# Performance work log

Hardware: AMD Instinct MI355X
Metric: run time of the kernel (lower is better)

Reference implementation:

```python
import jax, jax.numpy as jnp
import numpy as np

B, L, H, NH, HD, IT = 16, 512, 256, 8, 32, 2
NEG = -9e15


def _ln(x, g, b):
    m = x.mean(-1, keepdims=True)
    v = ((x - m) ** 2).mean(-1, keepdims=True)
    return (x - m) / jnp.sqrt(v + 1e-5) * g + b


def setup_inputs() -> dict:
    key = jax.random.key(0)
    ks = jax.random.split(key, 12)

    def nrm(k, shape, fan_in):
        return jax.random.normal(k, shape, dtype=jnp.float32) / np.float32(np.sqrt(fan_in))

    return {
        "data": jax.random.normal(ks[0], (B, L, H), jnp.float32),
        "gat_WQ_w": nrm(ks[1], (NH, H, H), H),
        "gat_WQ_b": jnp.zeros((NH, H), jnp.float32),
        "gat_a1": nrm(ks[2], (NH, 3 * H), 3 * H),
        "gat_a2": nrm(ks[3], (NH, 3 * H), 3 * H),
        "gat_fc_w": nrm(ks[4], (NH, 3 * H, HD), 3 * H),
        "gat_fc_b": jnp.zeros((NH, HD), jnp.float32),
        "norm_g": jnp.ones((IT, H), jnp.float32),
        "norm_b": jnp.zeros((IT, H), jnp.float32),
        "sq_w": nrm(ks[5], (IT, NH * HD, H), H),
        "sq_b": jnp.zeros((IT, NH * HD), jnp.float32),
        "sk_w": nrm(ks[6], (IT, NH * HD, H), H),
        "sk_b": jnp.zeros((IT, NH * HD), jnp.float32),
        "so_w": nrm(ks[7], (IT, H, NH * HD), NH * HD),
        "so_b": jnp.zeros((IT, H), jnp.float32),
        "fc_w": nrm(ks[8], (NH * HD, H), NH * HD),
        "fc_b": jnp.zeros((H,), jnp.float32),
        "mask": jax.random.randint(ks[9], (B, L), 0, 2, jnp.int32),
        "edge_matrix": jax.random.randint(ks[10], (B, L, L), 0, 2, jnp.int32),
    }


def _gat_head(xn, ax, adj_pos, Wq, bq, a1, a2, Fw, Fb):
    # xn: [B,L,H] normalized nodes; ax: [B,L,2H] interleaved (r_embs, relay)
    h = jnp.concatenate([xn @ Wq.T + bq, ax], axis=-1)  # [B,L,3H]
    # decomposed a^T [h_i ; h_j] = a1.h_i + a2.h_j  (avoids O(N^2*6H) concat)
    ei = h @ a1  # [B,L]
    ej = h @ a2  # [B,L]
    e = jax.nn.leaky_relu(ei[:, :, None] + ej[:, None, :], 0.2)  # [B,L,L]
    att = jax.nn.softmax(jnp.where(adj_pos, e, NEG), axis=2)
    hp = jnp.einsum('bij,bjd->bid', att, h)  # [B,L,3H]
    return jax.nn.elu(hp @ Fw + Fb)  # [B,L,HD]


def _forward(data, gat_WQ_w, gat_WQ_b, gat_a1, gat_a2, gat_fc_w, gat_fc_b,
             norm_g, norm_b, sq_w, sq_b, sk_w, sk_b, so_w, so_b, fc_w, fc_b,
             mask, edge_matrix):
    pad = mask == 0                                   # True at padding positions
    smask = jnp.concatenate([jnp.zeros((B, 1), bool), pad], axis=1)  # [B,L+1]
    adj_pos = edge_matrix > 0
    nodes = data                                      # [B,L,H]
    relay = data.mean(axis=1)                         # [B,H]
    gat = jax.vmap(_gat_head, in_axes=(None, None, None, 0, 0, 0, 0, 0, 0))
    scale = np.float32(1.0 / np.sqrt(HD))

    for i in range(IT):
        xn = _ln(nodes, norm_g[i], norm_b[i])
        # torch views [B,H,2,L] as [B,2H,L]: features interleave (r_embs, relay)
        ax = jnp.stack([data, jnp.broadcast_to(relay[:, None, :], (B, L, H))],
                       axis=-1).reshape(B, L, 2 * H)
        heads = gat(xn, ax, adj_pos, gat_WQ_w, gat_WQ_b, gat_a1, gat_a2,
                    gat_fc_w, gat_fc_b)               # [NH,B,L,HD]
        temp = jnp.transpose(heads, (1, 2, 0, 3)).reshape(B, L, NH * HD)
        nodes = nodes + jax.nn.leaky_relu(temp @ fc_w + fc_b, 0.01)
        # star attention (MSA2); note original uses v = k (WV unused)
        y = jnp.concatenate([relay[:, None, :], nodes], axis=1)   # [B,L+1,H]
        q = (relay @ sq_w[i].T + sq_b[i]).reshape(B, NH, HD)
        k = (y @ sk_w[i].T + sk_b[i]).transpose(0, 2, 1).reshape(B, NH, HD, L + 1)
        v = jnp.swapaxes(k, 2, 3)                                  # [B,NH,L+1,HD]
        pre = jnp.einsum('bnd,bndl->bnl', q, k) * scale
        pre = jnp.where(smask[:, None, :], -jnp.inf, pre)
        al = jax.nn.softmax(pre, axis=2)
        att = jnp.einsum('bnl,bnld->bnd', al, v).reshape(B, NH * HD)
        relay = jax.nn.leaky_relu(att @ so_w[i].T + so_b[i], 0.01)
        nodes = jnp.where(pad[:, :, None], 0.0, nodes)
    return nodes, relay


def reference(data, gat_WQ_w, gat_WQ_b, gat_a1, gat_a2, gat_fc_w, gat_fc_b,
              norm_g, norm_b, sq_w, sq_b, sk_w, sk_b, so_w, so_b, fc_w, fc_b,
              mask, edge_matrix):
    return _forward(data, gat_WQ_w, gat_WQ_b, gat_a1, gat_a2, gat_fc_w, gat_fc_b,
                    norm_g, norm_b, sq_w, sq_b, sk_w, sk_b, so_w, so_b, fc_w, fc_b,
                    mask, edge_matrix)
```

## Files before the change

kernel.cpp:

```cpp
#include <hip/hip_runtime.h>
#include <hip/hip_bf16.h>
#include <math.h>

#define BB 16
#define LL 512
#define HH 256
#define NHEAD 8
#define HDIM 32
#define LP1 513
#define NODES_ELEMS (BB*LL*HH)

typedef __attribute__((ext_vector_type(8))) short bf16x8;
typedef __attribute__((ext_vector_type(4))) float f32x4;

__device__ __forceinline__ unsigned short f2bf(float f) {
  union { float f; unsigned u; } x; x.f = f;
  unsigned r = x.u + 0x7fffu + ((x.u >> 16) & 1u);
  return (unsigned short)(r >> 16);
}
__device__ __forceinline__ float bf2f(unsigned short u) {
  union { unsigned u; float f; } x; x.u = (unsigned)u << 16; return x.f;
}

__global__ __launch_bounds__(256) void mega_prep_kernel(
    const float* __restrict__ data, const int* __restrict__ edge,
    const float* __restrict__ fc_w, const float* __restrict__ fcw,
    const float* __restrict__ sk_w, const float* __restrict__ sq_w,
    const float* __restrict__ so_w, const float* __restrict__ WQw,
    const float* __restrict__ WQb, const float* __restrict__ a1,
    const float* __restrict__ a2,
    unsigned short* __restrict__ datab, unsigned char* __restrict__ ep,
    unsigned short* __restrict__ fcwT, unsigned short* __restrict__ Bcat,
    unsigned short* __restrict__ skwb, float* __restrict__ sqT,
    float* __restrict__ soT, float* __restrict__ rpart,
    float* __restrict__ w1, float* __restrict__ w2,
    float* __restrict__ c1, float* __restrict__ c2,
    float* __restrict__ bqf, float* __restrict__ a1o, float* __restrict__ a2o) {
  int blk = blockIdx.x, t = threadIdx.x;
  if (blk < 2048) {
    int idx = blk * 1024 + t;
#pragma unroll
    for (int u = 0; u < 4; u++) { datab[idx] = f2bf(data[idx]); idx += 256; }
  } else if (blk < 4096) {
    int row = (blk - 2048) * 4 + (t >> 6);
    int lane = t & 63;
    const int* adj = edge + ((size_t)row << 9);
    unsigned v = 0;
#pragma unroll
    for (int u = 0; u < 8; u++) v |= (adj[lane + 64 * u] > 0 ? 1u : 0u) << u;
    ep[((size_t)row << 6) + lane] = (unsigned char)v;
  } else if (blk < 5120) {
    int b2 = blk - 4096;
    if (b2 < 256) {
      int idx = b2 * 256 + t;
      int o = idx >> 8, k = idx & 255;
      fcwT[idx] = f2bf(fc_w[k * 256 + o]);
    } else if (b2 < 512) {
      int idx = (b2 - 256) * 256 + t;
      int n = idx >> 13, d = (idx >> 8) & 31, c = idx & 255;
      Bcat[((size_t)n * 32 + d) * 512 + 256 + c] =
          f2bf(fcw[((size_t)n * 768 + 256 + 2 * c) * 32 + d]);
    } else {
      int idx = (b2 - 512) * 256 + t;
      skwb[idx] = f2bf(sk_w[idx]);
    }
  } else if (blk < 6144) {
    int q = blk - 5120;
    int which = q >> 8;
    const float* in = (which < 2) ? sq_w + which * 65536 : so_w + (which - 2) * 65536;
    float* out = (which < 2) ? sqT + which * 65536 : soT + (which - 2) * 65536;
    int idx = (q & 255) * 256 + t;
    int r = idx >> 8, c = idx & 255;
    out[c * 256 + r] = in[idx];
  } else if (blk < 6272) {
    int q = blk - 6144;
    int b = q >> 3, ch = q & 7;
    float s = 0.f;
    const float* p = data + ((size_t)b * 512 + ch * 64) * 256 + t;
    for (int l = 0; l < 64; l++) s += p[(size_t)l * 256];
    rpart[(size_t)q * 256 + t] = s;
  } else if (blk < 6280) {
    int n = blk - 6272;
    float s1 = 0.f, s2 = 0.f;
    for (int c = 0; c < 256; c++) {
      float wv = WQw[((size_t)(n * 256 + c)) * 256 + t];
      s1 = fmaf(a1[n * 768 + c], wv, s1);
      s2 = fmaf(a2[n * 768 + c], wv, s2);
    }
    w1[n * 256 + t] = s1;
    w2[n * 256 + t] = s2;
    if (t < 32) {
      float s = 0.f;
      for (int c = 0; c < 256; c++)
        s = fmaf(WQb[n * 256 + c], fcw[((size_t)n * 768 + c) * 32 + t], s);
      bqf[n * 32 + t] = s;
    }
    __shared__ float r1[256], r2[256];
    r1[t] = a1[n * 768 + t] * WQb[n * 256 + t];
    r2[t] = a2[n * 768 + t] * WQb[n * 256 + t];
    __syncthreads();
    for (int o = 128; o; o >>= 1) {
      if (t < o) { r1[t] += r1[t + o]; r2[t] += r2[t + o]; }
      __syncthreads();
    }
    if (t == 0) { c1[n] = r1[0]; c2[n] = r2[0]; }
  } else {
    int n = blk - 6280;
    a1o[n * 256 + t] = a1[n * 768 + 256 + 2 * t];
    a2o[n * 256 + t] = a2[n * 768 + 256 + 2 * t];
  }
}

__global__ __launch_bounds__(256) void bcat_m1_kernel(const float* __restrict__ WQw,
                                                      const float* __restrict__ fcw,
                                                      unsigned short* __restrict__ Bcat) {
  __shared__ float wq_s[256][16];
  __shared__ float fw_s[256][32];
  int n = blockIdx.x >> 4, kt = blockIdx.x & 15;
  int t = threadIdx.x;
#pragma unroll
  for (int i = 0; i < 16; i++) {
    int c = i * 16 + (t >> 4), kk = t & 15;
    wq_s[c][kk] = WQw[(size_t)n * 65536 + c * 256 + kt * 16 + kk];
  }
#pragma unroll
  for (int i = 0; i < 32; i++) {
    int idx = i * 256 + t;
    fw_s[idx >> 5][idx & 31] = fcw[(size_t)n * 24576 + idx];
  }
  __syncthreads();
  int kloc = t >> 4, dp = t & 15;
  float a0 = 0.f, a1v = 0.f;
  for (int c = 0; c < 256; c++) {
    float wv = wq_s[c][kloc];
    a0 = fmaf(wv, fw_s[c][dp * 2], a0);
    a1v = fmaf(wv, fw_s[c][dp * 2 + 1], a1v);
  }
  int k = kt * 16 + kloc;
  Bcat[((size_t)n * 32 + dp * 2) * 512 + k] = f2bf(a0);
  Bcat[((size_t)n * 32 + dp * 2 + 1) * 512 + k] = f2bf(a1v);
}

__device__ __forceinline__ void rarf_tail(
    int n, int b, int t, const float* rel,
    const float* __restrict__ a1, const float* __restrict__ a2,
    const float* __restrict__ fcw, const float* __restrict__ fcb,
    const float* __restrict__ bqf,
    float* __restrict__ ra1, float* __restrict__ ra2, float* __restrict__ rf,
    float* red1, float* red2, float* pf_s) {
  int lane = t & 63, w = t >> 6;
  float p1 = rel[t] * a1[n * 768 + 257 + 2 * t];
  float p2 = rel[t] * a2[n * 768 + 257 + 2 * t];
#pragma unroll
  for (int o = 32; o; o >>= 1) { p1 += __shfl_xor(p1, o); p2 += __shfl_xor(p2, o); }
  if (lane == 0) { red1[w] = p1; red2[w] = p2; }
  int d = t & 31, seg = t >> 5;
  float pf = 0.f;
  for (int u = 0; u < 32; u++) {
    int k = seg * 32 + u;
    pf = fmaf(rel[k], fcw[((size_t)n * 768 + 257 + 2 * k) * 32 + d], pf);
  }
  pf_s[seg * 33 + d] = pf;
  __syncthreads();
  if (t == 0) {
    ra1[n * 16 + b] = red1[0] + red1[1] + red1[2] + red1[3];
    ra2[n * 16 + b] = red2[0] + red2[1] + red2[2] + red2[3];
  }
  if (t < 32) {
    float s = 0.f;
    for (int gg = 0; gg < 8; gg++) s += pf_s[gg * 33 + t];
    rf[((size_t)n * 16 + b) * 32 + t] = s + fcb[n * 32 + t] + bqf[n * 32 + t];
  }
}

__global__ __launch_bounds__(256) void relay_rarf_kernel(
    const float* __restrict__ rpart,
    const unsigned short* __restrict__ skw0, const float* __restrict__ skb0,
    const float* __restrict__ a1, const float* __restrict__ a2,
    const float* __restrict__ fcw, const float* __restrict__ fcb,
    const float* __restrict__ bqf,
    float* __restrict__ relay, unsigned short* __restrict__ ktb,
    float* __restrict__ ra1, float* __restrict__ ra2, float* __restrict__ rf) {
  __shared__ float rel[256];
  __shared__ float red1[4], red2[4];
  __shared__ float pf_s[8 * 33];
  int n = blockIdx.x >> 4, b = blockIdx.x & 15;
  int t = threadIdx.x;
  float s = 0.f;
#pragma unroll
  for (int ch = 0; ch < 8; ch++) s += rpart[((size_t)(b * 8 + ch)) * 256 + t];
  s *= (1.0f / 512.0f);
  rel[t] = s;
  __syncthreads();
  if (n == 0) {
    relay[b * 256 + t] = s;
    float acc = 0.f;
    for (int k = 0; k < 256; k++) acc = fmaf(rel[k], bf2f(skw0[(size_t)t * 256 + k]), acc);
    ktb[((size_t)b * LP1) * 256 + t] = f2bf(acc + skb0[t]);
  }
  rarf_tail(n, b, t, rel, a1, a2, fcw, fcb, bqf, ra1, ra2, rf, red1, red2, pf_s);
}

__global__ __launch_bounds__(256) void so_rarf_kernel(
    const float* __restrict__ atts,
    const float* __restrict__ soT_it, const float* __restrict__ sob_it,
    const unsigned short* __restrict__ skw_nx, const float* __restrict__ skb_nx,
    const float* __restrict__ a1, const float* __restrict__ a2,
    const float* __restrict__ fcw, const float* __restrict__ fcb,
    const float* __restrict__ bqf, int do_extras,
    float* __restrict__ relay, unsigned short* __restrict__ ktb,
    float* __restrict__ ra1, float* __restrict__ ra2, float* __restrict__ rf) {
  int n = blockIdx.x >> 4, b = blockIdx.x & 15;
  if (!do_extras && n > 0) return;
  __shared__ float xr[256];
  __shared__ float rel[256];
  __shared__ float red1[4], red2[4];
  __shared__ float pf_s[8 * 33];
  int t = threadIdx.x;
  xr[t] = atts[b * 256 + t];
  __syncthreads();
  float acc = 0.f;
  for (int k = 0; k < 256; k++) acc = fmaf(xr[k], soT_it[(size_t)k * 256 + t], acc);
  float v = acc + sob_it[t];
  v = v > 0.f ? v : 0.01f * v;
  rel[t] = v;
  __syncthreads();
  if (n == 0) relay[b * 256 + t] = v;
  if (!do_extras) return;
  if (n == 0) {
    float a2v = 0.f;
    for (int k = 0; k < 256; k++) a2v = fmaf(rel[k], bf2f(skw_nx[(size_t)t * 256 + k]), a2v);
    ktb[((size_t)b * LP1) * 256 + t] = f2bf(a2v + skb_nx[t]);
  }
  rarf_tail(n, b, t, rel, a1, a2, fcw, fcb, bqf, ra1, ra2, rf, red1, red2, pf_s);
}

__global__ __launch_bounds__(256) void lnei_kernel(const float* __restrict__ src,
                                                   const unsigned short* __restrict__ datab,
                                                   const float* __restrict__ g,
                                                   const float* __restrict__ bb,
                                                   const float* __restrict__ w1,
                                                   const float* __restrict__ w2,
                                                   const float* __restrict__ a1o,
                                                   const float* __restrict__ a2o,
                                                   const float* __restrict__ c1,
                                                   const float* __restrict__ c2,
                                                   const float* __restrict__ ra1,
                                                   const float* __restrict__ ra2,
                                                   unsigned short* __restrict__ xnb,
                                                   float* __restrict__ ei,
                                                   float* __restrict__ ej) {
  int r = blockIdx.x * 4 + (threadIdx.x >> 6);
  int b = r >> 9;
  int lane = threadIdx.x & 63;
  float x[4], dv[4];
#pragma unroll
  for (int u = 0; u < 4; u++) {
    int c = lane + 64 * u;
    x[u] = src[(size_t)r * 256 + c];
    dv[u] = bf2f(datab[(size_t)r * 256 + c]);
  }
  float s = x[0] + x[1] + x[2] + x[3];
#pragma unroll
  for (int o = 32; o; o >>= 1) s += __shfl_xor(s, o);
  float mean = s * (1.0f / 256.0f);
  float v = 0.f;
#pragma unroll
  for (int u = 0; u < 4; u++) { x[u] -= mean; v = fmaf(x[u], x[u], v); }
#pragma unroll
  for (int o = 32; o; o >>= 1) v += __shfl_xor(v, o);
  float rstd = rsqrtf(v * (1.0f / 256.0f) + 1e-5f);
  float xv[4];
#pragma unroll
  for (int u = 0; u < 4; u++) {
    int c = lane + 64 * u;
    xv[u] = x[u] * rstd * g[c] + bb[c];
    xnb[(size_t)r * 256 + c] = f2bf(xv[u]);
  }
  float s1a[8], s2a[8];
#pragma unroll
  for (int n = 0; n < 8; n++) {
    float s1 = 0.f, s2 = 0.f;
#pragma unroll
    for (int u = 0; u < 4; u++) {
      int c = lane + 64 * u;
      s1 = fmaf(xv[u], w1[n * 256 + c], s1);
      s1 = fmaf(dv[u], a1o[n * 256 + c], s1);
      s2 = fmaf(xv[u], w2[n * 256 + c], s2);
      s2 = fmaf(dv[u], a2o[n * 256 + c], s2);
    }
    s1a[n] = s1; s2a[n] = s2;
  }
#pragma unroll
  for (int o = 32; o; o >>= 1) {
#pragma unroll
    for (int n = 0; n < 8; n++) {
      s1a[n] += __shfl_xor(s1a[n], o);
      s2a[n] += __shfl_xor(s2a[n], o);
    }
  }
  if (lane == 0) {
#pragma unroll
    for (int n = 0; n < 8; n++) {
      ei[n * 8192 + r] = s1a[n] + c1[n] + ra1[n * 16 + b];
      ej[n * 8192 + r] = s2a[n] + c2[n] + ra2[n * 16 + b];
    }
  }
}

__global__ __launch_bounds__(256) void g_gemm_kernel(
    const unsigned short* __restrict__ A1, const unsigned short* __restrict__ A2,
    const unsigned short* __restrict__ Bcat, unsigned short* __restrict__ GT) {
  int tileN = blockIdx.x * 64;
  int tileM = blockIdx.y * 128;
  int t = threadIdx.x;
  int wv = t >> 6, lane = t & 63;
  int lo = lane & 15, quad = lane >> 4;
  int rowBase0 = tileM + wv * 32;
  const unsigned short* ap1[2];
  const unsigned short* ap2[2];
#pragma unroll
  for (int rt = 0; rt < 2; rt++) {
    int arow = rowBase0 + rt * 16 + lo;
    ap1[rt] = A1 + (size_t)arow * 256 + quad * 8;
    ap2[rt] = A2 + (size_t)arow * 256 + quad * 8;
  }
  f32x4 acc[2][4] = {};
  for (int k0 = 0; k0 < 512; k0 += 32) {
    bf16x8 af[2];
#pragma unroll
    for (int rt = 0; rt < 2; rt++)
      af[rt] = (k0 < 256) ? *(const bf16x8*)(ap1[rt] + k0)
                          : *(const bf16x8*)(ap2[rt] + k0 - 256);
#pragma unroll
    for (int ct = 0; ct < 4; ct++) {
      bf16x8 bf_ = *(const bf16x8*)(Bcat + (size_t)(tileN + ct * 16 + lo) * 512 + k0 + quad * 8);
#pragma unroll
      for (int rt = 0; rt < 2; rt++)
        acc[rt][ct] = __builtin_amdgcn_mfma_f32_16x16x32_bf16(af[rt], bf_, acc[rt][ct], 0, 0, 0);
    }
  }
#pragma unroll
  for (int rt = 0; rt < 2; rt++) {
#pragma unroll
    for (int ct = 0; ct < 4; ct++) {
      int co = tileN + ct * 16 + lo;
      int n = co >> 5, d = co & 31;
      int jrow = rowBase0 + rt * 16 + quad * 4;
      int b2 = jrow >> 9, jj = jrow & 511;
      ushort4 pk;
      pk.x = f2bf(acc[rt][ct][0]);
      pk.y = f2bf(acc[rt][ct][1]);
      pk.z = f2bf(acc[rt][ct][2]);
      pk.w = f2bf(acc[rt][ct][3]);
      *(ushort4*)&GT[(((size_t)(n * 16 + b2) * 32 + d) << 9) + jj] = pk;
    }
  }
}

__global__ __launch_bounds__(256) void gat_agg_kernel(
    const unsigned short* __restrict__ GT,
    const float* __restrict__ ei, const float* __restrict__ ej,
    const unsigned char* __restrict__ ep,
    const float* __restrict__ rf,
    unsigned short* __restrict__ tempb) {
  __shared__ unsigned short W[32][512];
  __shared__ float denom_s[32];
  int blk = blockIdx.x;
  int n = blk >> 8;
  int b = (blk >> 4) & 15;
  int i0 = (blk & 15) << 5;
  int t = threadIdx.x;
  int wv = t >> 6, lane = t & 63;
  int lo = lane & 15, quad = lane >> 4;

  const float* ejrow = ej + n * 8192 + b * 512;
  float ejv[8];
#pragma unroll
  for (int u = 0; u < 8; u++) ejv[u] = ejrow[lane + 64 * u];
  float mm = ejv[0];
#pragma unroll
  for (int u = 1; u < 8; u++) mm = fmaxf(mm, ejv[u]);
#pragma unroll
  for (int o = 32; o; o >>= 1) mm = fmaxf(mm, __shfl_xor(mm, o));

  for (int rr = 0; rr < 8; rr++) {
    int row = wv * 8 + rr;
    float eiv = ei[n * 8192 + b * 512 + i0 + row];
    float M = eiv + mm;
    M = M > 0.f ? M : 0.2f * M;
    unsigned pb = ep[(((size_t)(b * 512 + i0 + row)) << 6) + lane];
    int rx = (row & 7) << 3;
#pragma unroll
    for (int u = 0; u < 8; u++) {
      float e = eiv + ejv[u];
      e = e > 0.f ? e : 0.2f * e;
      float w = ((pb >> u) & 1) ? __expf(e - M) : 0.f;
      int col = lane + 64 * u;
      W[row][((col >> 3 << 3) ^ rx) + (col & 7)] = f2bf(w);
    }
  }
  __syncthreads();

  int rt = wv >> 1, dh = wv & 1;
  int arow = rt * 16 + lo;
  int rx = arow & 7;
  const unsigned short* gtb = GT + (((size_t)(n * 16 + b) * 32) << 9);
  bf16x8 bones;
  {
    short ov = (lo == 0) ? (short)0x3F80 : (short)0;
#pragma unroll
    for (int j = 0; j < 8; j++) bones[j] = ov;
  }
  f32x4 acc = {}, accd = {};
  for (int k0 = 0; k0 < 512; k0 += 32) {
    int chunk = (k0 >> 3) + quad;
    bf16x8 a0 = *(const bf16x8*)&W[arow][(chunk ^ rx) << 3];
    bf16x8 bf_ = *(const bf16x8*)(gtb + (((size_t)(dh * 16 + lo)) << 9) + k0 + quad * 8);
    acc = __builtin_amdgcn_mfma_f32_16x16x32_bf16(a0, bf_, acc, 0, 0, 0);
    if (dh == 0)
      accd = __builtin_amdgcn_mfma_f32_16x16x32_bf16(a0, bones, accd, 0, 0, 0);
  }
  if (dh == 0 && lo == 0) {
#pragma unroll
    for (int r = 0; r < 4; r++) denom_s[rt * 16 + quad * 4 + r] = accd[r];
  }
  __syncthreads();
  int d = dh * 16 + lo;
  float base = rf[((size_t)n * 16 + b) * 32 + d];
#pragma unroll
  for (int r = 0; r < 4; r++) {
    int row = rt * 16 + quad * 4 + r;
    float inv = 1.0f / fmaxf(denom_s[row], 1e-35f);
    float v = acc[r] * inv + base;
    v = v > 0.f ? v : expm1f(v);
    tempb[((size_t)(b * 512 + i0 + row)) * 256 + n * 32 + d] = f2bf(v);
  }
}

__global__ __launch_bounds__(256) void fc_kt_kernel(
    const unsigned short* __restrict__ tempb,
    const unsigned short* __restrict__ fcwT,
    const float* __restrict__ fc_b,
    const unsigned short* __restrict__ skw_it,
    const float* __restrict__ skb_it,
    const int* __restrict__ mask,
    const float* __restrict__ resid,
    float* __restrict__ nodes,
    unsigned short* __restrict__ ktb) {
  __shared__ unsigned short tmp[32][264];
  int blk = blockIdx.x;
  int b = blk >> 4;
  int i0 = (blk & 15) << 5;
  int t = threadIdx.x;
  int wv = t >> 6, lane = t & 63;
  int lo = lane & 15, quad = lane >> 4;
  int ch = wv >> 1, rt2 = wv & 1;

  const unsigned short* arow_p = tempb + ((size_t)(b * 512 + i0 + rt2 * 16 + lo)) * 256 + quad * 8;
  f32x4 facc[8] = {};
  for (int k0 = 0; k0 < 256; k0 += 32) {
    bf16x8 a0 = *(const bf16x8*)(arow_p + k0);
#pragma unroll
    for (int ct = 0; ct < 8; ct++) {
      int co = ch * 128 + ct * 16 + lo;
      bf16x8 bf_ = *(const bf16x8*)(fcwT + (size_t)co * 256 + k0 + quad * 8);
      facc[ct] = __builtin_amdgcn_mfma_f32_16x16x32_bf16(a0, bf_, facc[ct], 0, 0, 0);
    }
  }
#pragma unroll
  for (int ct = 0; ct < 8; ct++) {
    int co = ch * 128 + ct * 16 + lo;
    float bv = fc_b[co];
#pragma unroll
    for (int r = 0; r < 4; r++) {
      int row = rt2 * 16 + quad * 4 + r;
      int grow = b * 512 + i0 + row;
      float v = facc[ct][r] + bv;
      v = v > 0.f ? v : 0.01f * v;
      v = (mask[grow] != 0) ? resid[(size_t)grow * 256 + co] + v : 0.f;
      nodes[(size_t)grow * 256 + co] = v;
      tmp[row][co] = f2bf(v);
    }
  }
  __syncthreads();

  f32x4 kacc[8] = {};
  for (int k0 = 0; k0 < 256; k0 += 32) {
    bf16x8 a0 = *(const bf16x8*)&tmp[rt2 * 16 + lo][k0 + quad * 8];
#pragma unroll
    for (int ct = 0; ct < 8; ct++) {
      int co = ch * 128 + ct * 16 + lo;
      bf16x8 bf_ = *(const bf16x8*)(skw_it + (size_t)co * 256 + k0 + quad * 8);
      kacc[ct] = __builtin_amdgcn_mfma_f32_16x16x32_bf16(a0, bf_, kacc[ct], 0, 0, 0);
    }
  }
#pragma unroll
  for (int ct = 0; ct < 8; ct++) {
    int co = ch * 128 + ct * 16 + lo;
    float bv = skb_it[co];
#pragma unroll
    for (int r = 0; r < 4; r++) {
      int row = rt2 * 16 + quad * 4 + r;
      int yrow = b * LP1 + 1 + i0 + row;
      ktb[(size_t)yrow * 256 + co] = f2bf(kacc[ct][r] + bv);
    }
  }
}

__global__ __launch_bounds__(256) void star_attn_kernel(const float* __restrict__ relay,
                                                        const float* __restrict__ sqT_it,
                                                        const float* __restrict__ sqb_it,
                                                        const unsigned short* __restrict__ ktb,
                                                        const int* __restrict__ mask,
                                                        float* __restrict__ attstar) {
  int b = blockIdx.x >> 3, n = blockIdx.x & 7;
  int t = threadIdx.x;
  int lane = t & 63, w = t >> 6;
  __shared__ float relb[256];
  __shared__ float qv[32];
  __shared__ float pre[LP1];
  __shared__ float red[4];
  __shared__ float par[8][33];
  relb[t] = relay[b * 256 + t];
  __syncthreads();
  {
    int d = t & 31, g = t >> 5;
    float qp = 0.f;
    for (int k = 0; k < 32; k++)
      qp = fmaf(relb[g * 32 + k], sqT_it[(size_t)(g * 32 + k) * 256 + n * 32 + d], qp);
    par[g][d] = qp;
  }
  __syncthreads();
  if (t < 32) {
    float q = 0.f;
#pragma unroll
    for (int gg = 0; gg < 8; gg++) q += par[gg][t];
    qv[t] = q + sqb_it[n * 32 + t];
  }
  __syncthreads();
  const float scale = 0.17677669529663687f;
  for (int l = t; l < LP1; l += 256) {
    bool masked = (l > 0) && (mask[b * LL + l - 1] == 0);
    float p;
    if (masked) p = -3.4e38f;
    else {
      p = 0.f;
      const unsigned short* krow = ktb + ((size_t)b * LP1 + l) * 256 + n * 32;
#pragma unroll
      for (int d = 0; d < 32; d++) p = fmaf(qv[d], bf2f(krow[d]), p);
      p *= scale;
    }
    pre[l] = p;
  }
  __syncthreads();
  float m = -3.4e38f;
  for (int l = t; l < LP1; l += 256) m = fmaxf(m, pre[l]);
#pragma unroll
  for (int o = 32; o; o >>= 1) m = fmaxf(m, __shfl_xor(m, o));
  if (lane == 0) red[w] = m;
  __syncthreads();
  m = fmaxf(fmaxf(red[0], red[1]), fmaxf(red[2], red[3]));
  __syncthreads();
  float s = 0.f;
  for (int l = t; l < LP1; l += 256) {
    float wv = __expf(pre[l] - m);
    pre[l] = wv;
    s += wv;
  }
#pragma unroll
  for (int o = 32; o; o >>= 1) s += __shfl_xor(s, o);
  if (lane == 0) red[w] = s;
  __syncthreads();
  float denom = red[0] + red[1] + red[2] + red[3];
  int d = t & 31, g = t >> 5;
  float acc = 0.f;
  for (int l = g; l < LP1; l += 8)
    acc = fmaf(pre[l], bf2f(ktb[((size_t)b * LP1 + l) * 256 + n * 32 + d]), acc);
  par[g][d] = acc;
  __syncthreads();
  if (t < 32) {
    float a = 0.f;
    for (int gg = 0; gg < 8; gg++) a += par[gg][t];
    attstar[b * 256 + n * 32 + t] = a / denom;
  }
}

extern "C" void kernel_launch(void* const* d_in, const int* in_sizes, int n_in,
                              void* d_out, int out_size, void* d_ws, size_t ws_size,
                              hipStream_t stream) {
  const float* data  = (const float*)d_in[0];
  const float* WQw   = (const float*)d_in[1];
  const float* WQb   = (const float*)d_in[2];
  const float* a1    = (const float*)d_in[3];
  const float* a2    = (const float*)d_in[4];
  const float* fcw_g = (const float*)d_in[5];
  const float* fcb_g = (const float*)d_in[6];
  const float* ng    = (const float*)d_in[7];
  const float* nb    = (const float*)d_in[8];
  const float* sq_w  = (const float*)d_in[9];
  const float* sq_b  = (const float*)d_in[10];
  const float* sk_w  = (const float*)d_in[11];
  const float* sk_b  = (const float*)d_in[12];
  const float* so_w  = (const float*)d_in[13];
  const float* so_b  = (const float*)d_in[14];
  const float* fc_w  = (const float*)d_in[15];
  const float* fc_b  = (const float*)d_in[16];
  const int*   mask  = (const int*)d_in[17];
  const int*   edge  = (const int*)d_in[18];

  float* nodes = (float*)d_out;
  float* relay = nodes + NODES_ELEMS;

  char* p = (char*)d_ws;
  auto alloc = [&](size_t bytes) -> char* {
    char* r = p; p += (bytes + 255) & ~(size_t)255; return r;
  };
  unsigned short* xnb  = (unsigned short*)alloc((size_t)8192 * 256 * 2);
  unsigned short* datab= (unsigned short*)alloc((size_t)8192 * 256 * 2);
  unsigned short* GT   = (unsigned short*)alloc((size_t)8 * 16 * 32 * 512 * 2);
  unsigned short* tmpb = (unsigned short*)alloc((size_t)8192 * 256 * 2);
  unsigned short* ktb  = (unsigned short*)alloc((size_t)8208 * 256 * 2);
  unsigned char* ep    = (unsigned char*)alloc((size_t)8192 * 64);
  float* ei            = (float*)alloc(65536 * 4);
  float* ej            = (float*)alloc(65536 * 4);
  float* ra1           = (float*)alloc(128 * 4);
  float* ra2           = (float*)alloc(128 * 4);
  float* rf            = (float*)alloc(4096 * 4);
  float* bqf           = (float*)alloc(256 * 4);
  float* w1            = (float*)alloc(2048 * 4);
  float* w2            = (float*)alloc(2048 * 4);
  float* c1            = (float*)alloc(8 * 4);
  float* c2            = (float*)alloc(8 * 4);
  float* a1o           = (float*)alloc(2048 * 4);
  float* a2o           = (float*)alloc(2048 * 4);
  float* rpart         = (float*)alloc(128 * 256 * 4);
  unsigned short* Bcat = (unsigned short*)alloc((size_t)256 * 512 * 2);
  unsigned short* fcwT = (unsigned short*)alloc((size_t)65536 * 2);
  unsigned short* skwb = (unsigned short*)alloc((size_t)131072 * 2);
  float* sqT           = (float*)alloc((size_t)131072 * 4);
  float* soT           = (float*)alloc((size_t)131072 * 4);
  float* atts          = (float*)alloc(4096 * 4);

  mega_prep_kernel<<<6288, 256, 0, stream>>>(data, edge, fc_w, fcw_g, sk_w, sq_w,
                                             so_w, WQw, WQb, a1, a2,
                                             datab, ep, fcwT, Bcat, skwb, sqT, soT,
                                             rpart, w1, w2, c1, c2, bqf, a1o, a2o);
  bcat_m1_kernel<<<128, 256, 0, stream>>>(WQw, fcw_g, Bcat);
  relay_rarf_kernel<<<128, 256, 0, stream>>>(rpart, skwb, sk_b, a1, a2, fcw_g,
                                             fcb_g, bqf, relay, ktb, ra1, ra2, rf);

  for (int it = 0; it < 2; it++) {
    const float* src = (it == 0) ? data : nodes;
    lnei_kernel<<<2048, 256, 0, stream>>>(src, datab, ng + it * 256, nb + it * 256,
                                          w1, w2, a1o, a2o, c1, c2, ra1, ra2,
                                          xnb, ei, ej);
    g_gemm_kernel<<<dim3(4, 64), 256, 0, stream>>>(xnb, datab, Bcat, GT);
    gat_agg_kernel<<<NHEAD * BB * 16, 256, 0, stream>>>(GT, ei, ej, ep, rf, tmpb);
    fc_kt_kernel<<<256, 256, 0, stream>>>(tmpb, fcwT, fc_b,
                                          skwb + it * 65536, sk_b + it * 256,
                                          mask, src, nodes, ktb);
    star_attn_kernel<<<BB * NHEAD, 256, 0, stream>>>(relay, sqT + it * 65536,
                                                     sq_b + it * 256, ktb, mask, atts);
    so_rarf_kernel<<<128, 256, 0, stream>>>(atts, soT + it * 65536, so_b + it * 256,
                                            skwb + 65536, sk_b + 256,
                                            a1, a2, fcw_g, fcb_g, bqf,
                                            (it == 0) ? 1 : 0,
                                            relay, ktb, ra1, ra2, rf);
  }
}
```

Baseline: 386.3 us.

## Restructure prep kernel: fuse data cast with relay sum, tile transposes, split reductions

The one-time prep kernel is reorganised. The bf16 cast of data is fused with the per-chunk relay row sums so data is read once. Weight transposes now go through a padded 64x64 shared-memory tile so reads and writes are coalesced, and the Bcat fill index order is changed for coalesced reads. The serial 256-iteration reductions for w1/w2, bqf and c1/c2 are split across more blocks and threads with shared-memory partial sums. The grid shrinks from 6288 to 3162 blocks; the fused cast path has fewer, longer-running blocks, which risks lower parallelism for that part.

```diff
diff --git a/kernel.cpp b/kernel.cpp
--- a/kernel.cpp
+++ b/kernel.cpp
@@ -36,78 +36,125 @@
     float* __restrict__ w1, float* __restrict__ w2,
     float* __restrict__ c1, float* __restrict__ c2,
     float* __restrict__ bqf, float* __restrict__ a1o, float* __restrict__ a2o) {
+  __shared__ float smem[64 * 65];
   int blk = blockIdx.x, t = threadIdx.x;
-  if (blk < 2048) {
-    int idx = blk * 1024 + t;
-#pragma unroll
-    for (int u = 0; u < 4; u++) { datab[idx] = f2bf(data[idx]); idx += 256; }
-  } else if (blk < 4096) {
-    int row = (blk - 2048) * 4 + (t >> 6);
+  if (blk < 128) {
+    int b = blk >> 3, ch = blk & 7;
+    const float* pr = data + ((size_t)b * 512 + ch * 64) * 256 + t;
+    unsigned short* db = datab + ((size_t)b * 512 + ch * 64) * 256 + t;
+    float s = 0.f;
+    for (int l = 0; l < 64; l++) {
+      float v = pr[(size_t)l * 256];
+      db[(size_t)l * 256] = f2bf(v);
+      s += v;
+    }
+    rpart[(size_t)blk * 256 + t] = s;
+  } else if (blk < 2176) {
+    int row = (blk - 128) * 4 + (t >> 6);
     int lane = t & 63;
     const int* adj = edge + ((size_t)row << 9);
     unsigned v = 0;
 #pragma unroll
     for (int u = 0; u < 8; u++) v |= (adj[lane + 64 * u] > 0 ? 1u : 0u) << u;
     ep[((size_t)row << 6) + lane] = (unsigned char)v;
-  } else if (blk < 5120) {
-    int b2 = blk - 4096;
-    if (b2 < 256) {
-      int idx = b2 * 256 + t;
-      int o = idx >> 8, k = idx & 255;
-      fcwT[idx] = f2bf(fc_w[k * 256 + o]);
-    } else if (b2 < 512) {
-      int idx = (b2 - 256) * 256 + t;
-      int n = idx >> 13, d = (idx >> 8) & 31, c = idx & 255;
-      Bcat[((size_t)n * 32 + d) * 512 + 256 + c] =
-          f2bf(fcw[((size_t)n * 768 + 256 + 2 * c) * 32 + d]);
-    } else {
-      int idx = (b2 - 512) * 256 + t;
-      skwb[idx] = f2bf(sk_w[idx]);
-    }
-  } else if (blk < 6144) {
-    int q = blk - 5120;
-    int which = q >> 8;
-    const float* in = (which < 2) ? sq_w + which * 65536 : so_w + (which - 2) * 65536;
-    float* out = (which < 2) ? sqT + which * 65536 : soT + (which - 2) * 65536;
-    int idx = (q & 255) * 256 + t;
-    int r = idx >> 8, c = idx & 255;
-    out[c * 256 + r] = in[idx];
-  } else if (blk < 6272) {
-    int q = blk - 6144;
-    int b = q >> 3, ch = q & 7;
-    float s = 0.f;
-    const float* p = data + ((size_t)b * 512 + ch * 64) * 256 + t;
-    for (int l = 0; l < 64; l++) s += p[(size_t)l * 256];
-    rpart[(size_t)q * 256 + t] = s;
-  } else if (blk < 6280) {
-    int n = blk - 6272;
+  } else if (blk < 2432) {
+    int idx = (blk - 2176) * 256 + t;
+    int d = idx & 31;
+    int g = idx >> 5;
+    int n = g >> 8, c = g & 255;
+    Bcat[((size_t)n * 32 + d) * 512 + 256 + c] =
+        f2bf(fcw[((size_t)n * 768 + 256 + 2 * c) * 32 + d]);
+  } else if (blk < 2944) {
+    int idx = (blk - 2432) * 256 + t;
+    skwb[idx] = f2bf(sk_w[idx]);
+  } else if (blk < 3024) {
+    int q = blk - 2944;
+    int mat = q >> 4, tl = q & 15;
+    int r0 = (tl >> 2) * 64, c0 = (tl & 3) * 64;
+    const float* in;
+    if (mat == 0) in = fc_w;
+    else if (mat <= 2) in = sq_w + (mat - 1) * 65536;
+    else in = so_w + (mat - 3) * 65536;
+    int cc = t & 63, rq = t >> 6;
+#pragma unroll
+    for (int i = 0; i < 16; i++) {
+      int r = rq + i * 4;
+      smem[r * 65 + cc] = in[(r0 + r) * 256 + c0 + cc];
+    }
+    __syncthreads();
+#pragma unroll
+    for (int i = 0; i < 16; i++) {
+      int cp = rq + i * 4;
+      float v = smem[cc * 65 + cp];
+      if (mat == 0) fcwT[(c0 + cp) * 256 + r0 + cc] = f2bf(v);
+      else if (mat <= 2) sqT[(mat - 1) * 65536 + (c0 + cp) * 256 + r0 + cc] = v;
+      else soT[(mat - 3) * 65536 + (c0 + cp) * 256 + r0 + cc] = v;
+    }
+  } else if (blk < 3152) {
+    int q = blk - 3024;
+    int n = q >> 4, kc = q & 15;
+    int k = kc * 16 + (t & 15), cseg = t >> 4;
     float s1 = 0.f, s2 = 0.f;
-    for (int c = 0; c < 256; c++) {
-      float wv = WQw[((size_t)(n * 256 + c)) * 256 + t];
+#pragma unroll
+    for (int u = 0; u < 16; u++) {
+      int c = cseg * 16 + u;
+      float wv = WQw[((size_t)(n * 256 + c)) * 256 + k];
       s1 = fmaf(a1[n * 768 + c], wv, s1);
       s2 = fmaf(a2[n * 768 + c], wv, s2);
     }
-    w1[n * 256 + t] = s1;
-    w2[n * 256 + t] = s2;
-    if (t < 32) {
-      float s = 0.f;
-      for (int c = 0; c < 256; c++)
-        s = fmaf(WQb[n * 256 + c], fcw[((size_t)n * 768 + c) * 32 + t], s);
-      bqf[n * 32 + t] = s;
-    }
-    __shared__ float r1[256], r2[256];
-    r1[t] = a1[n * 768 + t] * WQb[n * 256 + t];
-    r2[t] = a2[n * 768 + t] * WQb[n * 256 + t];
+    smem[cseg * 16 + (t & 15)] = s1;
+    smem[256 + cseg * 16 + (t & 15)] = s2;
     __syncthreads();
-    for (int o = 128; o; o >>= 1) {
-      if (t < o) { r1[t] += r1[t + o]; r2[t] += r2[t + o]; }
-      __syncthreads();
-    }
-    if (t == 0) { c1[n] = r1[0]; c2[n] = r2[0]; }
+    if (cseg == 0) {
+      float a = 0.f, b2 = 0.f;
+#pragma unroll
+      for (int u = 0; u < 16; u++) {
+        a += smem[u * 16 + (t & 15)];
+        b2 += smem[256 + u * 16 + (t & 15)];
+      }
+      w1[n * 256 + k] = a;
+      w2[n * 256 + k] = b2;
+    }
+  } else if (blk < 3160) {
+    int n = blk - 3152;
+    int d = t & 31, seg = t >> 5;
+    float s = 0.f;
+#pragma unroll
+    for (int u = 0; u < 32; u++) {
+      int c = seg * 32 + u;
+      s = fmaf(WQb[n * 256 + c], fcw[((size_t)n * 768 + c) * 32 + d], s);
+    }
+    smem[seg * 32 + d] = s;
+    __syncthreads();
+    if (seg == 0) {
+      float a = 0.f;
+#pragma unroll
+      for (int u = 0; u < 8; u++) a += smem[u * 32 + d];
+      bqf[n * 32 + d] = a;
+    }
+  } else if (blk == 3160) {
+    int n = t >> 5, sl = t & 31;
+    float s1 = 0.f, s2 = 0.f;
+#pragma unroll
+    for (int u = 0; u < 8; u++) {
+      int c = sl * 8 + u;
+      float wb = WQb[n * 256 + c];
+      s1 = fmaf(a1[n * 768 + c], wb, s1);
+      s2 = fmaf(a2[n * 768 + c], wb, s2);
+    }
+    smem[t] = s1; smem[256 + t] = s2;
+    __syncthreads();
+    if (sl == 0) {
+      float a = 0.f, b2 = 0.f;
+      for (int u = 0; u < 32; u++) { a += smem[n * 32 + u]; b2 += smem[256 + n * 32 + u]; }
+      c1[n] = a; c2[n] = b2;
+    }
   } else {
-    int n = blk - 6280;
-    a1o[n * 256 + t] = a1[n * 768 + 256 + 2 * t];
-    a2o[n * 256 + t] = a2[n * 768 + 256 + 2 * t];
+#pragma unroll
+    for (int n = 0; n < 8; n++) {
+      a1o[n * 256 + t] = a1[n * 768 + 256 + 2 * t];
+      a2o[n * 256 + t] = a2[n * 768 + 256 + 2 * t];
+    }
   }
 }
 
@@ -642,7 +689,7 @@
   float* soT           = (float*)alloc((size_t)131072 * 4);
   float* atts          = (float*)alloc(4096 * 4);
 
-  mega_prep_kernel<<<6288, 256, 0, stream>>>(data, edge, fc_w, fcw_g, sk_w, sq_w,
+  mega_prep_kernel<<<3162, 256, 0, stream>>>(data, edge, fc_w, fcw_g, sk_w, sq_w,
                                              so_w, WQw, WQb, a1, a2,
                                              datab, ep, fcwT, Bcat, skwb, sqT, soT,
                                              rpart, w1, w2, c1, c2, bqf, a1o, a2o);
```

After: 363.6 us. 5.9% less time.
